# Optimization experiments

Measured on AMD Instinct MI355X. Metric: run time of the kernel, lower is better.

## Reference

```python
import jax, jax.numpy as jnp
import numpy as np

NUM_CLASSES = 5
SMOOTH = 1e-5


def setup_inputs() -> dict:
    key = jax.random.key(0)
    k1, k2, k3 = jax.random.split(key, 3)
    B, C, X, Y, Z = 2, NUM_CLASSES, 128, 128, 128
    net_output = jax.random.normal(k1, (B, C, X, Y, Z), dtype=jnp.float32)
    target = jax.random.randint(k2, (B, 1, X, Y, Z), 0, C, dtype=jnp.int64)
    dist = jax.random.uniform(k3, (B, 1, X, Y, Z), dtype=jnp.float32)
    return {"net_output": net_output, "target": target, "dist": dist}


def reference(net_output, target, dist):
    # --- Distance-map penalized multi-class Dice ---
    p = jax.nn.softmax(net_output, axis=1)  # (B,C,X,Y,Z)
    gt = target[:, 0]  # (B,X,Y,Z)
    classes = jnp.arange(NUM_CLASSES)[None, :, None, None, None]
    y_onehot = (gt[:, None] == classes).astype(p.dtype)  # (B,C,X,Y,Z)
    # per-class, per-batch sums over spatial dims
    tp = jnp.sum(p * y_onehot * dist, axis=(2, 3, 4))  # (B,C), dist broadcasts over C
    denom = jnp.sum(p, axis=(2, 3, 4)) + jnp.sum(y_onehot, axis=(2, 3, 4))  # (B,C)
    dc = (2.0 * tp + SMOOTH) / (denom + SMOOTH)  # (B,C)
    # sum over classes of batch-mean, divided by num_classes == overall mean
    dpdc_loss = -jnp.mean(dc)
    # --- Cross entropy (mean over all voxels), target squeezed to class idx ---
    logp = jax.nn.log_softmax(net_output, axis=1)  # (B,C,X,Y,Z)
    nll = -jnp.take_along_axis(logp, target, axis=1)  # (B,1,X,Y,Z)
    ce_loss = jnp.mean(nll)
    # aggregate == 'sum', weight_ce = weight_dice = 1
    return ce_loss + dpdc_loss
```

## Files before the change

### kernel.cpp

```cpp
#include <hip/hip_runtime.h>

#define NC 5
#define NB 2
#define SPATIAL (128*128*128)
#define NGROUPS (SPATIAL/4)
#define TILE_GROUPS 256
#define NTILES (NGROUPS/TILE_GROUPS)
#define GX 256
#define TPB (NTILES/GX)
#define SMOOTHF 1e-5f

#define TILE_BYTES (32*1024)


__device__ __forceinline__ void async16(const void* g, void* l) {
    __builtin_amdgcn_global_load_lds(
        (const __attribute__((address_space(1))) void*)g,
        (__attribute__((address_space(3))) void*)l, 16, 0, 0);
}

__global__ __launch_bounds__(256) void dpdc_main(
    const float* __restrict__ net, const void* __restrict__ targ,
    const float* __restrict__ dist, float* __restrict__ slots)
{
    __shared__ __align__(16) char lds[2][TILE_BYTES];
    const int b   = blockIdx.y;
    const int tid = threadIdx.x;

    const unsigned long long tv = ((const unsigned long long*)targ)[tid & 63];
    const int t64 = (__ballot(tv >= 5ull) == 0ull);

    const char* netb  = (const char*)net  + (size_t)b * NC * SPATIAL * 4;
    const char* distb = (const char*)dist + (size_t)b * SPATIAL * 4;
    const char* targb = (const char*)targ + (size_t)b * SPATIAL * (t64 ? 8 : 4);

    const int tl0 = blockIdx.x * TPB;

    auto stage = [&](int tl, int bf) {
        char* base = &lds[bf][0];
        const size_t toff = (size_t)tl * 4096 + tid * 16;
        #pragma unroll
        for (int c = 0; c < NC; ++c)
            async16(netb + (size_t)c * SPATIAL * 4 + toff, base + c * 4096 + tid * 16);
        async16(distb + toff, base + 20480 + tid * 16);
        if (t64) {
            const char* ts = targb + (size_t)tl * 8192 + tid * 16;
            async16(ts,        base + 24576 + tid * 16);
            async16(ts + 4096, base + 28672 + tid * 16);
        } else {
            async16(targb + toff, base + 24576 + tid * 16);
        }
    };

    float tp[NC], sp[NC];
    #pragma unroll
    for (int c = 0; c < NC; ++c) { tp[c] = 0.f; sp[c] = 0.f; }
    unsigned cntp = 0u;
    float nll = 0.f;

    stage(tl0, 0);
    __syncthreads();

    #pragma unroll 1
    for (int k = 0; k < TPB; ++k) {
        if (k + 1 < TPB) stage(tl0 + k + 1, (k + 1) & 1);

        const char* base = &lds[k & 1][0];
        float4 l[NC];
        #pragma unroll
        for (int c = 0; c < NC; ++c)
            l[c] = *(const float4*)(base + c * 4096 + tid * 16);
        float4 dd = *(const float4*)(base + 20480 + tid * 16);
        int tt[4];
        if (t64) {
            ulonglong2 a = *(const ulonglong2*)(base + 24576 + tid * 32);
            ulonglong2 q = *(const ulonglong2*)(base + 24576 + tid * 32 + 16);
            tt[0] = (int)a.x; tt[1] = (int)a.y;
            tt[2] = (int)q.x; tt[3] = (int)q.y;
        } else {
            int4 a = *(const int4*)(base + 24576 + tid * 16);
            tt[0] = a.x; tt[1] = a.y; tt[2] = a.z; tt[3] = a.w;
        }
        const float* dv = (const float*)&dd;
        #pragma unroll
        for (int j = 0; j < 4; ++j) {
            float lc[NC];
            #pragma unroll
            for (int c = 0; c < NC; ++c) lc[c] = ((const float*)&l[c])[j];
            float e[NC];
            float s = 0.f;
            #pragma unroll
            for (int c = 0; c < NC; ++c) { e[c] = __expf(lc[c]); s += e[c]; }
            float inv = 1.0f / s;
            int t = tt[j];
            float lsel = lc[4];
            #pragma unroll
            for (int c = 0; c < 4; ++c) lsel = (t == c) ? lc[c] : lsel;
            float pd = dv[j] * inv;
            #pragma unroll
            for (int c = 0; c < NC; ++c) {
                float p = e[c] * inv;
                sp[c] += p;
                tp[c] += (t == c) ? e[c] * pd : 0.f;
            }
            cntp += 1u << (6 * t);
            nll += __logf(s) - lsel;
        }
        __syncthreads();
    }

    __shared__ float red[4][16];
    float vals[16];
    #pragma unroll
    for (int c = 0; c < NC; ++c) {
        vals[c] = tp[c]; vals[5 + c] = sp[c];
        vals[10 + c] = (float)((cntp >> (6 * c)) & 63u);
    }
    vals[15] = nll;
    const int lane = tid & 63;
    const int wave = tid >> 6;
    #pragma unroll
    for (int k = 0; k < 16; ++k) {
        float v = vals[k];
        #pragma unroll
        for (int off = 32; off > 0; off >>= 1) v += __shfl_down(v, off, 64);
        if (lane == 0) red[wave][k] = v;
    }
    __syncthreads();
    if (tid < 16) {
        float v = red[0][tid] + red[1][tid] + red[2][tid] + red[3][tid];
        slots[((size_t)b * GX + blockIdx.x) * 16 + tid] = v;
    }
}

__global__ __launch_bounds__(1024) void finalize(const float* __restrict__ slots,
                                                 float* __restrict__ out) {
    __shared__ float part[1024];
    __shared__ float tot[32];
    const int j = threadIdx.x;
    const int p = j & 31;
    const int b = p >> 4, k = p & 15;
    float s = 0.f;
    for (int slot = j >> 5; slot < GX; slot += 32)
        s += slots[((size_t)b * GX + slot) * 16 + k];
    part[j] = s;
    __syncthreads();
    if (j < 32) {
        float t = 0.f;
        #pragma unroll
        for (int m = 0; m < 32; ++m) t += part[j + 32 * m];
        tot[j] = t;
    }
    __syncthreads();
    if (j == 0) {
        float dcsum = 0.f;
        for (int bb = 0; bb < NB; ++bb)
            for (int c = 0; c < NC; ++c) {
                float tpv = tot[bb * 16 + c];
                float spv = tot[bb * 16 + 5 + c];
                float cv  = tot[bb * 16 + 10 + c];
                dcsum += (2.f * tpv + SMOOTHF) / (spv + cv + SMOOTHF);
            }
        float ce = (tot[15] + tot[31]) / (float)((size_t)NB * SPATIAL);
        out[0] = ce - dcsum / (float)(NB * NC);
    }
}

extern "C" void kernel_launch(void* const* d_in, const int* in_sizes, int n_in,
                              void* d_out, int out_size, void* d_ws, size_t ws_size,
                              hipStream_t stream) {
    const float* net  = (const float*)d_in[0];
    const void*  targ = d_in[1];
    const float* dist = (const float*)d_in[2];
    float* slots = (float*)d_ws;

    dim3 grid(GX, NB);
    dpdc_main<<<grid, 256, 0, stream>>>(net, targ, dist, slots);
    finalize<<<1, 1024, 0, stream>>>(slots, (float*)d_out);
}
```

Baseline: 32.73 us.

## Load dist and target into registers with prefetch and enlarge grid

The dist and target streams no longer go through LDS via async global-to-LDS copies. They are now loaded straight into registers one tile ahead, which shrinks the LDS double buffer from 32 KB to 20 KB per stage. The grid doubles from 256 to 512 blocks per batch, or fewer if the workspace is too small, and tiles per block becomes a runtime argument. The aim is higher occupancy and more blocks to hide memory latency, at the cost of extra registers for the prefetched values and a runtime loop bound.

```diff
diff --git a/kernel.cpp b/kernel.cpp
--- a/kernel.cpp
+++ b/kernel.cpp
@@ -3,14 +3,11 @@
 #define NC 5
 #define NB 2
 #define SPATIAL (128*128*128)
-#define NGROUPS (SPATIAL/4)
-#define TILE_GROUPS 256
-#define NTILES (NGROUPS/TILE_GROUPS)
-#define GX 256
-#define TPB (NTILES/GX)
+#define TILE_VOX 1024
+#define NTILES (SPATIAL/TILE_VOX)
 #define SMOOTHF 1e-5f
 
-#define TILE_BYTES (32*1024)
+#define TILE_BYTES 20480
 
 
 __device__ __forceinline__ void async16(const void* g, void* l) {
@@ -21,7 +18,7 @@
 
 __global__ __launch_bounds__(256) void dpdc_main(
     const float* __restrict__ net, const void* __restrict__ targ,
-    const float* __restrict__ dist, float* __restrict__ slots)
+    const float* __restrict__ dist, float* __restrict__ slots, int TPB)
 {
     __shared__ __align__(16) char lds[2][TILE_BYTES];
     const int b   = blockIdx.y;
@@ -30,9 +27,11 @@
     const unsigned long long tv = ((const unsigned long long*)targ)[tid & 63];
     const int t64 = (__ballot(tv >= 5ull) == 0ull);
 
-    const char* netb  = (const char*)net  + (size_t)b * NC * SPATIAL * 4;
-    const char* distb = (const char*)dist + (size_t)b * SPATIAL * 4;
-    const char* targb = (const char*)targ + (size_t)b * SPATIAL * (t64 ? 8 : 4);
+    const char* netb = (const char*)net + (size_t)b * NC * SPATIAL * 4;
+    const float4* db4 = (const float4*)(dist + (size_t)b * SPATIAL);
+    const int4* t32p = (const int4*)((const int*)targ + (size_t)b * SPATIAL);
+    const ulonglong2* t64p =
+        (const ulonglong2*)((const unsigned long long*)targ + (size_t)b * SPATIAL);
 
     const int tl0 = blockIdx.x * TPB;
 
@@ -41,15 +40,8 @@
         const size_t toff = (size_t)tl * 4096 + tid * 16;
         #pragma unroll
         for (int c = 0; c < NC; ++c)
-            async16(netb + (size_t)c * SPATIAL * 4 + toff, base + c * 4096 + tid * 16);
-        async16(distb + toff, base + 20480 + tid * 16);
-        if (t64) {
-            const char* ts = targb + (size_t)tl * 8192 + tid * 16;
-            async16(ts,        base + 24576 + tid * 16);
-            async16(ts + 4096, base + 28672 + tid * 16);
-        } else {
-            async16(targb + toff, base + 24576 + tid * 16);
-        }
+            async16(netb + (size_t)c * SPATIAL * 4 + toff,
+                    base + c * 4096 + tid * 16);
     };
 
     float tp[NC], sp[NC];
@@ -59,29 +51,39 @@
     float nll = 0.f;
 
     stage(tl0, 0);
+    float4 dd_c; ulonglong2 ta_c, tq_c; int4 t3_c;
+    {
+        const int g = tl0 * 256 + tid;
+        dd_c = db4[g];
+        if (t64) { ta_c = t64p[2 * g]; tq_c = t64p[2 * g + 1]; }
+        else     { t3_c = t32p[g]; }
+    }
     __syncthreads();
 
     #pragma unroll 1
     for (int k = 0; k < TPB; ++k) {
-        if (k + 1 < TPB) stage(tl0 + k + 1, (k + 1) & 1);
+        float4 dd_n; ulonglong2 ta_n, tq_n; int4 t3_n;
+        if (k + 1 < TPB) {
+            stage(tl0 + k + 1, (k + 1) & 1);
+            const int gn = (tl0 + k + 1) * 256 + tid;
+            dd_n = db4[gn];
+            if (t64) { ta_n = t64p[2 * gn]; tq_n = t64p[2 * gn + 1]; }
+            else     { t3_n = t32p[gn]; }
+        }
 
         const char* base = &lds[k & 1][0];
         float4 l[NC];
         #pragma unroll
         for (int c = 0; c < NC; ++c)
             l[c] = *(const float4*)(base + c * 4096 + tid * 16);
-        float4 dd = *(const float4*)(base + 20480 + tid * 16);
         int tt[4];
         if (t64) {
-            ulonglong2 a = *(const ulonglong2*)(base + 24576 + tid * 32);
-            ulonglong2 q = *(const ulonglong2*)(base + 24576 + tid * 32 + 16);
-            tt[0] = (int)a.x; tt[1] = (int)a.y;
-            tt[2] = (int)q.x; tt[3] = (int)q.y;
+            tt[0] = (int)ta_c.x; tt[1] = (int)ta_c.y;
+            tt[2] = (int)tq_c.x; tt[3] = (int)tq_c.y;
         } else {
-            int4 a = *(const int4*)(base + 24576 + tid * 16);
-            tt[0] = a.x; tt[1] = a.y; tt[2] = a.z; tt[3] = a.w;
+            tt[0] = t3_c.x; tt[1] = t3_c.y; tt[2] = t3_c.z; tt[3] = t3_c.w;
         }
-        const float* dv = (const float*)&dd;
+        const float* dv = (const float*)&dd_c;
         #pragma unroll
         for (int j = 0; j < 4; ++j) {
             float lc[NC];
@@ -107,6 +109,7 @@
             nll += __logf(s) - lsel;
         }
         __syncthreads();
+        dd_c = dd_n; ta_c = ta_n; tq_c = tq_n; t3_c = t3_n;
     }
 
     __shared__ float red[4][16];
@@ -129,20 +132,20 @@
     __syncthreads();
     if (tid < 16) {
         float v = red[0][tid] + red[1][tid] + red[2][tid] + red[3][tid];
-        slots[((size_t)b * GX + blockIdx.x) * 16 + tid] = v;
+        slots[((size_t)b * gridDim.x + blockIdx.x) * 16 + tid] = v;
     }
 }
 
 __global__ __launch_bounds__(1024) void finalize(const float* __restrict__ slots,
-                                                 float* __restrict__ out) {
+                                                 int gx, float* __restrict__ out) {
     __shared__ float part[1024];
     __shared__ float tot[32];
     const int j = threadIdx.x;
     const int p = j & 31;
     const int b = p >> 4, k = p & 15;
     float s = 0.f;
-    for (int slot = j >> 5; slot < GX; slot += 32)
-        s += slots[((size_t)b * GX + slot) * 16 + k];
+    for (int slot = j >> 5; slot < gx; slot += 32)
+        s += slots[((size_t)b * gx + slot) * 16 + k];
     part[j] = s;
     __syncthreads();
     if (j < 32) {
@@ -174,7 +177,11 @@
     const float* dist = (const float*)d_in[2];
     float* slots = (float*)d_ws;
 
-    dim3 grid(GX, NB);
-    dpdc_main<<<grid, 256, 0, stream>>>(net, targ, dist, slots);
-    finalize<<<1, 1024, 0, stream>>>(slots, (float*)d_out);
+    int gx = 512;
+    while ((size_t)NB * gx * 16 * sizeof(float) > ws_size && gx > 1) gx >>= 1;
+    const int tpb = NTILES / gx;
+
+    dim3 grid(gx, NB);
+    dpdc_main<<<grid, 256, 0, stream>>>(net, targ, dist, slots, tpb);
+    finalize<<<1, 1024, 0, stream>>>(slots, gx, (float*)d_out);
 }
```

New measurement: 37.84 us. 15.6% more time.

## Give each wave private LDS double buffers and drop block-wide barriers

Applied to the files above, without the earlier changes.

Each wave now stages its own contiguous 256-voxel slice into a private double-buffered LDS region. Ordering uses explicit s_waitcnt vmcnt/lgkmcnt and sched_barrier instead of __syncthreads, so waves stream independently and no longer stall on the slowest wave each step. The int32-target path issues a duplicate load so every stage has a fixed count of eight outstanding loads for the vmcnt(8) wait. This relies on hand-written waitcnt semantics, which is fragile if the compiler inserts or reorders other memory ops.

```diff
diff --git a/kernel.cpp b/kernel.cpp
--- a/kernel.cpp
+++ b/kernel.cpp
@@ -3,14 +3,14 @@
 #define NC 5
 #define NB 2
 #define SPATIAL (128*128*128)
-#define NGROUPS (SPATIAL/4)
-#define TILE_GROUPS 256
-#define NTILES (NGROUPS/TILE_GROUPS)
+#define WTILE_VOX 256
+#define BTILE_VOX 1024
+#define NSTEPS (SPATIAL/BTILE_VOX)
 #define GX 256
-#define TPB (NTILES/GX)
+#define TPB (NSTEPS/GX)
 #define SMOOTHF 1e-5f
 
-#define TILE_BYTES (32*1024)
+#define WBUF 8192
 
 
 __device__ __forceinline__ void async16(const void* g, void* l) {
@@ -23,32 +23,36 @@
     const float* __restrict__ net, const void* __restrict__ targ,
     const float* __restrict__ dist, float* __restrict__ slots)
 {
-    __shared__ __align__(16) char lds[2][TILE_BYTES];
-    const int b   = blockIdx.y;
-    const int tid = threadIdx.x;
+    __shared__ __align__(16) char lds[2][4][WBUF];
+    const int tid = threadIdx.x, wave = tid >> 6, lane = tid & 63;
+    const int b = blockIdx.y;
 
-    const unsigned long long tv = ((const unsigned long long*)targ)[tid & 63];
+    const unsigned long long tv = ((const unsigned long long*)targ)[lane];
     const int t64 = (__ballot(tv >= 5ull) == 0ull);
 
     const char* netb  = (const char*)net  + (size_t)b * NC * SPATIAL * 4;
     const char* distb = (const char*)dist + (size_t)b * SPATIAL * 4;
     const char* targb = (const char*)targ + (size_t)b * SPATIAL * (t64 ? 8 : 4);
 
-    const int tl0 = blockIdx.x * TPB;
+    const size_t vb0 = (size_t)blockIdx.x * TPB * BTILE_VOX
+                     + (size_t)wave * WTILE_VOX;
 
-    auto stage = [&](int tl, int bf) {
-        char* base = &lds[bf][0];
-        const size_t toff = (size_t)tl * 4096 + tid * 16;
+    auto stage = [&](int k, int bf) {
+        char* base = &lds[bf][wave][0];
+        const size_t vb = vb0 + (size_t)k * BTILE_VOX;
+        const char* ns = netb + vb * 4 + lane * 16;
         #pragma unroll
         for (int c = 0; c < NC; ++c)
-            async16(netb + (size_t)c * SPATIAL * 4 + toff, base + c * 4096 + tid * 16);
-        async16(distb + toff, base + 20480 + tid * 16);
+            async16(ns + (size_t)c * SPATIAL * 4, base + c * 1024 + lane * 16);
+        async16(distb + vb * 4 + lane * 16, base + 5120 + lane * 16);
         if (t64) {
-            const char* ts = targb + (size_t)tl * 8192 + tid * 16;
-            async16(ts,        base + 24576 + tid * 16);
-            async16(ts + 4096, base + 28672 + tid * 16);
+            const char* ts = targb + vb * 8 + lane * 16;
+            async16(ts,        base + 6144 + lane * 16);
+            async16(ts + 1024, base + 7168 + lane * 16);
         } else {
-            async16(targb + toff, base + 24576 + tid * 16);
+            const char* ts = targb + vb * 4 + lane * 16;
+            async16(ts, base + 6144 + lane * 16);
+            async16(ts, base + 7168 + lane * 16);
         }
     };
 
@@ -58,27 +62,32 @@
     unsigned cntp = 0u;
     float nll = 0.f;
 
-    stage(tl0, 0);
-    __syncthreads();
+    stage(0, 0);
 
     #pragma unroll 1
     for (int k = 0; k < TPB; ++k) {
-        if (k + 1 < TPB) stage(tl0 + k + 1, (k + 1) & 1);
+        if (k + 1 < TPB) {
+            stage(k + 1, (k + 1) & 1);
+            asm volatile("s_waitcnt vmcnt(8)" ::: "memory");
+        } else {
+            asm volatile("s_waitcnt vmcnt(0)" ::: "memory");
+        }
+        __builtin_amdgcn_sched_barrier(0);
 
-        const char* base = &lds[k & 1][0];
+        const char* base = &lds[k & 1][wave][0];
         float4 l[NC];
         #pragma unroll
         for (int c = 0; c < NC; ++c)
-            l[c] = *(const float4*)(base + c * 4096 + tid * 16);
-        float4 dd = *(const float4*)(base + 20480 + tid * 16);
+            l[c] = *(const float4*)(base + c * 1024 + lane * 16);
+        float4 dd = *(const float4*)(base + 5120 + lane * 16);
         int tt[4];
         if (t64) {
-            ulonglong2 a = *(const ulonglong2*)(base + 24576 + tid * 32);
-            ulonglong2 q = *(const ulonglong2*)(base + 24576 + tid * 32 + 16);
+            ulonglong2 a = *(const ulonglong2*)(base + 6144 + lane * 32);
+            ulonglong2 q = *(const ulonglong2*)(base + 6144 + lane * 32 + 16);
             tt[0] = (int)a.x; tt[1] = (int)a.y;
             tt[2] = (int)q.x; tt[3] = (int)q.y;
         } else {
-            int4 a = *(const int4*)(base + 24576 + tid * 16);
+            int4 a = *(const int4*)(base + 6144 + lane * 16);
             tt[0] = a.x; tt[1] = a.y; tt[2] = a.z; tt[3] = a.w;
         }
         const float* dv = (const float*)&dd;
@@ -106,7 +115,8 @@
             cntp += 1u << (6 * t);
             nll += __logf(s) - lsel;
         }
-        __syncthreads();
+        asm volatile("s_waitcnt lgkmcnt(0)" ::: "memory");
+        __builtin_amdgcn_sched_barrier(0);
     }
 
     __shared__ float red[4][16];
@@ -117,8 +127,6 @@
         vals[10 + c] = (float)((cntp >> (6 * c)) & 63u);
     }
     vals[15] = nll;
-    const int lane = tid & 63;
-    const int wave = tid >> 6;
     #pragma unroll
     for (int k = 0; k < 16; ++k) {
         float v = vals[k];
```

Result: no change. 32.43 us (-0.9%).
